# Kernel tuning notes

Hardware: AMD Instinct MI355X
Metric: run time of the kernel (lower is better)

The kernel has to match this reference:

```python
import jax, jax.numpy as jnp
import numpy as np

B, S, E = 4, 2048, 1024
H = 16
D = E // H
WIN = 512


def setup_inputs() -> dict:
    key = jax.random.key(0)
    k1, k2, k3 = jax.random.split(key, 3)
    x = jax.random.normal(k1, (B, S, E), dtype=jnp.float32)
    w_in = jax.random.normal(k2, (3 * E, E), dtype=jnp.float32) * 0.02
    w_out = jax.random.normal(k3, (E, E), dtype=jnp.float32) * 0.02
    return {"x": x, "w_in": w_in, "w_out": w_out}


def _sliding_window_attention(q, k, v, win):
    b, h, s, d = q.shape
    nb = s // win
    scale = 1.0 / jnp.sqrt(jnp.float32(d))
    qb = q.reshape(b, h, nb, win, d)
    kb = k.reshape(b, h, nb, win, d)
    vb = v.reshape(b, h, nb, win, d)
    zpad = jnp.zeros_like(kb[:, :, :1])
    k2 = jnp.concatenate([jnp.concatenate([zpad, kb[:, :, :-1]], axis=2), kb], axis=3)  # [B,H,nb,2W,D]
    v2 = jnp.concatenate([jnp.concatenate([zpad, vb[:, :, :-1]], axis=2), vb], axis=3)
    scores = jnp.einsum('bhnqd,bhnkd->bhnqk', qb, k2) * scale  # [B,H,nb,W,2W]
    qi = jnp.arange(win)[:, None]          # query offset in block
    kj = jnp.arange(2 * win)[None, :]
    delta = qi - kj + win                  # q_idx - kv_idx
    valid = (delta >= 0) & (delta <= win)  # sliding-window causal mask
    blk = jnp.arange(nb)[:, None, None]
    valid = valid[None] & (blk * win + (kj[None] - win) >= 0)  # prev block invalid for block 0
    # ALiBi: bias = (q_idx - kv_idx) * exp2(-(h+1)*8/H)
    slopes = jnp.exp2(-(jnp.arange(H, dtype=jnp.float32) + 1.0) * 8.0 / H)  # [H]
    bias = slopes[:, None, None] * delta.astype(jnp.float32)  # [H,W,2W]
    scores = jnp.where(valid[None, :, :, :, :][:, None].squeeze(0)[None] if False else valid[None, None],
                       scores + bias[None, :, None], -jnp.inf)
    p = jax.nn.softmax(scores, axis=-1)
    out = jnp.einsum('bhnqk,bhnkd->bhnqd', p, v2)
    return out.reshape(b, h, s, d)


def reference(x, w_in, w_out):
    b, s, e = x.shape
    # packed in-projection (q is k is v path): split [3E,E] weight
    qkv = jnp.einsum('bse,fe->bsf', x, w_in)  # [B,S,3E]
    q, k, v = jnp.split(qkv, 3, axis=-1)
    def heads(t):
        return t.reshape(b, s, H, D).transpose(0, 2, 1, 3)  # [B,H,S,D]
    o = _sliding_window_attention(heads(q), heads(k), heads(v), WIN)  # [B,H,S,D]
    o = o.transpose(0, 2, 1, 3).reshape(b, s, e)
    return jnp.einsum('bse,fe->bsf', o, w_out)  # out_proj, batch-first output
```

## Files before the change

### kernel.cpp

```cpp
#include <hip/hip_runtime.h>
#include <hip/hip_bf16.h>


typedef __bf16 bf16x8 __attribute__((ext_vector_type(8)));
typedef float f32x4 __attribute__((ext_vector_type(4)));

__device__ __forceinline__ f32x4 mfma16(bf16x8 a, bf16x8 b, f32x4 c) {
    return __builtin_amdgcn_mfma_f32_16x16x32_bf16(a, b, c, 0, 0, 0);
}

__device__ __forceinline__ void gload_lds16(const void* g, void* l) {
    __builtin_amdgcn_global_load_lds(
        (const __attribute__((address_space(1))) unsigned int*)(unsigned long long)g,
        (__attribute__((address_space(3))) unsigned int*)(unsigned int)(unsigned long long)l,
        16, 0, 0);
}

__device__ __forceinline__ unsigned pkbf(float a, float b) {
    unsigned short ua = __builtin_bit_cast(unsigned short, (__bf16)a);
    unsigned short ub = __builtin_bit_cast(unsigned short, (__bf16)b);
    return (unsigned)ua | ((unsigned)ub << 16);
}

__global__ void init_flag(int* flag) { *flag = 0; }

__global__ void detect_f32(const unsigned short* __restrict__ w, int n, int* flag) {
    int i = blockIdx.x * blockDim.x + threadIdx.x;
    int hit = 0;
    for (; i < n; i += gridDim.x * blockDim.x) {
        int e = (w[i] >> 7) & 0xFF;
        if (e >= 0x8D) hit = 1;
    }
    unsigned long long m = __ballot(hit);
    if (m != 0 && (threadIdx.x & 63) == 0) atomicOr(flag, 1);
}

__global__ void cvt_all(const void* __restrict__ x, const void* __restrict__ wi,
                        const void* __restrict__ wo, __bf16* __restrict__ xb,
                        __bf16* __restrict__ wib, __bf16* __restrict__ wob,
                        const int* __restrict__ flag) {
    if (*flag == 0) return;
    const int XN = 8192 * 1024, WI = 3072 * 1024, WO = 1024 * 1024;
    const int stride = gridDim.x * blockDim.x;
    int i0 = blockIdx.x * blockDim.x + threadIdx.x;
    for (int j = i0; j < XN; j += stride) xb[j] = (__bf16)((const float*)x)[j];
    for (int j = i0; j < WI; j += stride) wib[j] = (__bf16)((const float*)wi)[j];
    for (int j = i0; j < WO; j += stride) wob[j] = (__bf16)((const float*)wo)[j];
}

__global__ __launch_bounds__(256, 3) void gemm_bt(
        const void* __restrict__ Araw, const __bf16* __restrict__ Acvt,
        const void* __restrict__ Braw, const __bf16* __restrict__ Bcvt,
        __bf16* __restrict__ Cb, float* __restrict__ Cf,
        const int* __restrict__ flagp, int M, int N, int K) {
    __shared__ __align__(16) __bf16 As[128 * 64];
    __shared__ __align__(16) __bf16 Bs[128 * 64];

    const int t = threadIdx.x;
    const int lane = t & 63;
    const int w = t >> 6;
    const int wr = w >> 1, wc = w & 1;
    const int q4 = lane >> 4, l16 = lane & 15;
    const int m0 = blockIdx.y * 128, n0 = blockIdx.x * 128;
    const bool isf32 = (*flagp != 0);
    const __bf16* A = isf32 ? Acvt : (const __bf16*)Araw;
    const __bf16* Bt = isf32 ? Bcvt : (const __bf16*)Braw;

    f32x4 acc[4][4] = {};

    const int lr = lane >> 3;
    const int lc = (lane & 7) ^ lr;

    for (int k0 = 0; k0 < K; k0 += 64) {
#pragma unroll
        for (int p = 0; p < 4; ++p) {
            int r0 = w * 32 + p * 8;
            gload_lds16(&A[(size_t)(m0 + r0 + lr) * K + k0 + lc * 8], &As[r0 * 64]);
            gload_lds16(&Bt[(size_t)(n0 + r0 + lr) * K + k0 + lc * 8], &Bs[r0 * 64]);
        }
        __syncthreads();

#pragma unroll
        for (int kt = 0; kt < 2; ++kt) {
            bf16x8 af[4], bfr[4];
#pragma unroll
            for (int mt = 0; mt < 4; ++mt) {
                int row = wr * 64 + mt * 16 + l16;
                af[mt] = *(const bf16x8*)&As[row * 64 + (((kt * 4 + q4) ^ (row & 7)) << 3)];
            }
#pragma unroll
            for (int nt = 0; nt < 4; ++nt) {
                int row = wc * 64 + nt * 16 + l16;
                bfr[nt] = *(const bf16x8*)&Bs[row * 64 + (((kt * 4 + q4) ^ (row & 7)) << 3)];
            }
#pragma unroll
            for (int mt = 0; mt < 4; ++mt)
#pragma unroll
                for (int nt = 0; nt < 4; ++nt)
                    acc[mt][nt] = mfma16(af[mt], bfr[nt], acc[mt][nt]);
        }
        __syncthreads();
    }

#pragma unroll
    for (int mt = 0; mt < 4; ++mt)
#pragma unroll
        for (int nt = 0; nt < 4; ++nt) {
            int col = n0 + wc * 64 + nt * 16 + l16;
#pragma unroll
            for (int r = 0; r < 4; ++r) {
                int row = m0 + wr * 64 + mt * 16 + q4 * 4 + r;
                if (Cf && isf32)
                    Cf[(size_t)row * N + col] = acc[mt][nt][r];
                else
                    Cb[(size_t)row * N + col] = (__bf16)acc[mt][nt][r];
            }
        }
}

__global__ __launch_bounds__(256, 2) void attn(
        const __bf16* __restrict__ qkv, __bf16* __restrict__ o) {
    __shared__ __align__(16) char smem[52224];
    __bf16* Ks  = (__bf16*)smem;
    __bf16* Vts = (__bf16*)(smem + 16384);
    __bf16* Ps  = (__bf16*)(smem + 33792);
    __bf16* Ot  = (__bf16*)smem;

    const int qt = blockIdx.x, h = blockIdx.y, b = blockIdx.z;
    const int t = threadIdx.x;
    const int lane = t & 63, w = t >> 6;
    const int q4 = lane >> 4, l16 = lane & 15;
    const int q0 = qt * 128, qw0 = q0 + w * 32;

    const float L2E = 1.4426950408889634f;
    const float slope2 = exp2f(-(float)(h + 1) * 0.5f) * L2E;
    const float scale2 = L2E * 0.125f;

    const int srow = t >> 3, scb = t & 7;
    const int ksoff = (scb ^ (srow & 7)) << 3;

    bf16x8 qf[2][2];
    const size_t qbase = ((size_t)b * 2048 + q0) * 3072 + (size_t)h * 64;
#pragma unroll
    for (int nt = 0; nt < 2; ++nt)
#pragma unroll
        for (int kt = 0; kt < 2; ++kt)
            qf[nt][kt] = *(const bf16x8*)&qkv[qbase +
                (size_t)(w * 32 + nt * 16 + l16) * 3072 + kt * 32 + q4 * 8];

    f32x4 O[4][2] = {};
    float mrow[2] = {-1e30f, -1e30f}, lrow[2] = {0.0f, 0.0f};

    const int nkt = (qt < 4 ? qt : 4) + 1;
    const int ktile0 = qt - (nkt - 1);
    const size_t bh = (size_t)b * 2048 * 3072 + (size_t)h * 64;

    uint4 kpre[4], vpre[4];

    {
        const size_t kb = bh + (size_t)(ktile0 * 128) * 3072 + 1024;
#pragma unroll
        for (int p = 0; p < 4; ++p)
            kpre[p] = *(const uint4*)&qkv[kb + (size_t)(p * 32 + srow) * 3072 + scb * 8];
#pragma unroll
        for (int p = 0; p < 4; ++p)
            vpre[p] = *(const uint4*)&qkv[kb + 1024 + (size_t)(p * 32 + srow) * 3072 + scb * 8];
#pragma unroll
        for (int p = 0; p < 4; ++p) {
            *(uint4*)&Ks[(p * 32 + srow) * 64 + ksoff] = kpre[p];
            const __bf16* ve = (const __bf16*)&vpre[p];
            int R = p * 4 + (srow >> 3);
#pragma unroll
            for (int j = 0; j < 8; ++j)
                Vts[(scb * 8 + j) * 136 + ((R ^ scb) << 3) + (srow & 7)] = ve[j];
        }
    }
    __syncthreads();

    for (int ki = 0; ki < nkt; ++ki) {
        const int k0 = (ktile0 + ki) * 128;
        if (ki + 1 < nkt) {
            const size_t kb = bh + (size_t)(k0 + 128) * 3072 + 1024;
#pragma unroll
            for (int p = 0; p < 4; ++p)
                kpre[p] = *(const uint4*)&qkv[kb + (size_t)(p * 32 + srow) * 3072 + scb * 8];
#pragma unroll
            for (int p = 0; p < 4; ++p)
                vpre[p] = *(const uint4*)&qkv[kb + 1024 + (size_t)(p * 32 + srow) * 3072 + scb * 8];
        }

#pragma unroll 1
        for (int hh = 0; hh < 2; ++hh) {
            const int ks0 = k0 + hh * 64;
            if (qw0 + 31 < ks0 || qw0 - 512 > ks0 + 63) continue;

            f32x4 sc[2][4] = {};
#pragma unroll
            for (int mt = 0; mt < 4; ++mt) {
                int krow = hh * 64 + mt * 16 + l16;
                bf16x8 ak0 = *(const bf16x8*)&Ks[krow * 64 + ((q4 ^ (l16 & 7)) << 3)];
                bf16x8 ak1 = *(const bf16x8*)&Ks[krow * 64 + (((4 + q4) ^ (l16 & 7)) << 3)];
                sc[0][mt] = mfma16(ak0, qf[0][0], sc[0][mt]);
                sc[0][mt] = mfma16(ak1, qf[0][1], sc[0][mt]);
                sc[1][mt] = mfma16(ak0, qf[1][0], sc[1][mt]);
                sc[1][mt] = mfma16(ak1, qf[1][1], sc[1][mt]);
            }

            float al[2];
#pragma unroll
            for (int nt = 0; nt < 2; ++nt) {
                const int qi = qw0 + nt * 16 + l16;
                const int db = qi - ks0 - q4 * 4;
                float tmx = -1e30f;
#pragma unroll
                for (int mt = 0; mt < 4; ++mt)
#pragma unroll
                    for (int r = 0; r < 4; ++r) {
                        int delta = db - mt * 16 - r;
                        float v = sc[nt][mt][r] * scale2 + slope2 * (float)delta;
                        v = ((unsigned)delta <= 512u) ? v : -1e30f;
                        sc[nt][mt][r] = v;
                        tmx = fmaxf(tmx, v);
                    }
                tmx = fmaxf(tmx, __shfl_xor(tmx, 16));
                tmx = fmaxf(tmx, __shfl_xor(tmx, 32));
                float mnew = fmaxf(mrow[nt], tmx);
                al[nt] = exp2f(mrow[nt] - mnew);
                mrow[nt] = mnew;
#pragma unroll
                for (int mtd = 0; mtd < 4; ++mtd)
                    O[mtd][nt] *= al[nt];
            }

            float rsum[2] = {0.0f, 0.0f};
#pragma unroll
            for (int nt = 0; nt < 2; ++nt) {
                int qrow = w * 32 + nt * 16 + l16;
#pragma unroll
                for (int mt = 0; mt < 4; ++mt) {
                    float p0 = exp2f(sc[nt][mt][0] - mrow[nt]);
                    float p1 = exp2f(sc[nt][mt][1] - mrow[nt]);
                    float p2 = exp2f(sc[nt][mt][2] - mrow[nt]);
                    float p3 = exp2f(sc[nt][mt][3] - mrow[nt]);
                    rsum[nt] += (p0 + p1) + (p2 + p3);
                    uint2 pk;
                    pk.x = pkbf(p0, p1);
                    pk.y = pkbf(p2, p3);
                    *(uint2*)&Ps[qrow * 72 + mt * 16 + q4 * 4] = pk;
                }
            }

#pragma unroll
            for (int kt = 0; kt < 2; ++kt) {
                bf16x8 bp0 = *(const bf16x8*)&Ps[(w * 32 + l16) * 72 + kt * 32 + q4 * 8];
                bf16x8 bp1 = *(const bf16x8*)&Ps[(w * 32 + 16 + l16) * 72 + kt * 32 + q4 * 8];
#pragma unroll
                for (int mtd = 0; mtd < 4; ++mtd) {
                    int d = mtd * 16 + l16;
                    int kb2 = (hh * 8 + kt * 4 + q4) ^ ((mtd * 2 + (l16 >> 3)) & 7);
                    bf16x8 av = *(const bf16x8*)&Vts[d * 136 + (kb2 << 3)];
                    O[mtd][0] = mfma16(av, bp0, O[mtd][0]);
                    O[mtd][1] = mfma16(av, bp1, O[mtd][1]);
                }
            }
#pragma unroll
            for (int nt = 0; nt < 2; ++nt) {
                float rs = rsum[nt];
                rs += __shfl_xor(rs, 16);
                rs += __shfl_xor(rs, 32);
                lrow[nt] = lrow[nt] * al[nt] + rs;
            }
        }

        __syncthreads();
        if (ki + 1 < nkt) {
#pragma unroll
            for (int p = 0; p < 4; ++p) {
                *(uint4*)&Ks[(p * 32 + srow) * 64 + ksoff] = kpre[p];
                const __bf16* ve = (const __bf16*)&vpre[p];
                int R = p * 4 + (srow >> 3);
#pragma unroll
                for (int j = 0; j < 8; ++j)
                    Vts[(scb * 8 + j) * 136 + ((R ^ scb) << 3) + (srow & 7)] = ve[j];
            }
        }
        __syncthreads();
    }

#pragma unroll
    for (int nt = 0; nt < 2; ++nt) {
        float inv = (lrow[nt] > 0.0f) ? 1.0f / lrow[nt] : 0.0f;
        int qrow = w * 32 + nt * 16 + l16;
#pragma unroll
        for (int mtd = 0; mtd < 4; ++mtd) {
            int chunk = (mtd * 2 + (q4 >> 1)) ^ (l16 & 7);
            uint2 pk;
            pk.x = pkbf(O[mtd][nt][0] * inv, O[mtd][nt][1] * inv);
            pk.y = pkbf(O[mtd][nt][2] * inv, O[mtd][nt][3] * inv);
            *(uint2*)&Ot[qrow * 64 + (chunk << 3) + (q4 & 1) * 4] = pk;
        }
    }
    const size_t obase = ((size_t)b * 2048 + q0) * 1024 + (size_t)h * 64;
#pragma unroll
    for (int i = 0; i < 4; ++i) {
        int u = i * 64 + lane;
        int row = u >> 3, ch = u & 7;
        int q = w * 32 + row;
        *(uint4*)&o[obase + (size_t)q * 1024 + ch * 8] =
            *(const uint4*)&Ot[q * 64 + ((ch ^ (row & 7)) << 3)];
    }
}

extern "C" void kernel_launch(void* const* d_in, const int* in_sizes, int n_in,
                              void* d_out, int out_size, void* d_ws, size_t ws_size,
                              hipStream_t stream) {
    char* ws = (char*)d_ws;
    int* flag = (int*)ws;
    size_t off = 256;
    __bf16* xb  = (__bf16*)(ws + off); off += (size_t)8192 * 1024 * 2;
    __bf16* wib = (__bf16*)(ws + off); off += (size_t)3072 * 1024 * 2;
    __bf16* wob = (__bf16*)(ws + off); off += (size_t)1024 * 1024 * 2;
    __bf16* qkv = (__bf16*)(ws + off); off += (size_t)8192 * 3072 * 2;
    __bf16* o   = (__bf16*)(ws + off);

    init_flag<<<1, 1, 0, stream>>>(flag);
    int nscan = in_sizes[2] < 65536 ? in_sizes[2] : 65536;
    detect_f32<<<16, 256, 0, stream>>>((const unsigned short*)d_in[2], nscan, flag);
    cvt_all<<<1024, 256, 0, stream>>>(d_in[0], d_in[1], d_in[2], xb, wib, wob, flag);

    gemm_bt<<<dim3(24, 64), 256, 0, stream>>>(d_in[0], xb, d_in[1], wib,
                                              qkv, nullptr, flag, 8192, 3072, 1024);
    attn<<<dim3(16, 16, 4), 256, 0, stream>>>(qkv, o);
    gemm_bt<<<dim3(8, 64), 256, 0, stream>>>(o, o, d_in[2], wob,
                                             (__bf16*)d_out, (float*)d_out, flag,
                                             8192, 1024, 1024);
}
```

Before: 266.7 us.

## Write V transposed from QKV GEMM epilogue and reverse attention tile order

The QKV projection GEMM epilogue now writes the V columns straight into a per-head transposed [B,H,D,S] buffer, while Q and K go into a narrower [B*S,2048] buffer. The attention kernel can then load V^T rows with plain 16-byte loads and stores into shared memory, instead of the old scalar transpose scatter of 8 bf16 values per lane. Attention blocks are also launched in reverse query-tile order so the tiles with the most KV work are scheduled first. The cost is that the GEMM epilogue writes V with a strided pattern, 8-byte stores per lane at a 2048-element stride, which may hurt write coalescing.

```diff
diff --git a/kernel.cpp b/kernel.cpp
--- a/kernel.cpp
+++ b/kernel.cpp
@@ -52,7 +52,8 @@
         const void* __restrict__ Araw, const __bf16* __restrict__ Acvt,
         const void* __restrict__ Braw, const __bf16* __restrict__ Bcvt,
         __bf16* __restrict__ Cb, float* __restrict__ Cf,
-        const int* __restrict__ flagp, int M, int N, int K) {
+        __bf16* __restrict__ vTp, const int* __restrict__ flagp,
+        int M, int N, int K, int ldc) {
     __shared__ __align__(16) __bf16 As[128 * 64];
     __shared__ __align__(16) __bf16 Bs[128 * 64];
 
@@ -102,31 +103,49 @@
         __syncthreads();
     }
 
-#pragma unroll
-    for (int mt = 0; mt < 4; ++mt)
-#pragma unroll
-        for (int nt = 0; nt < 4; ++nt) {
-            int col = n0 + wc * 64 + nt * 16 + l16;
-#pragma unroll
-            for (int r = 0; r < 4; ++r) {
-                int row = m0 + wr * 64 + mt * 16 + q4 * 4 + r;
-                if (Cf && isf32)
-                    Cf[(size_t)row * N + col] = acc[mt][nt][r];
-                else
-                    Cb[(size_t)row * N + col] = (__bf16)acc[mt][nt][r];
-            }
-        }
+    if (vTp && n0 >= 2048) {
+        const int b = m0 >> 11;
+        const int s0 = (m0 & 2047) + wr * 64 + q4 * 4;
+#pragma unroll
+        for (int mt = 0; mt < 4; ++mt)
+#pragma unroll
+            for (int nt = 0; nt < 4; ++nt) {
+                int dg = n0 - 2048 + wc * 64 + nt * 16 + l16;
+                size_t base = ((size_t)(b * 16 + (dg >> 6)) * 64 + (dg & 63)) * 2048 +
+                              s0 + mt * 16;
+                uint2 pk;
+                pk.x = pkbf(acc[mt][nt][0], acc[mt][nt][1]);
+                pk.y = pkbf(acc[mt][nt][2], acc[mt][nt][3]);
+                *(uint2*)&vTp[base] = pk;
+            }
+    } else {
+#pragma unroll
+        for (int mt = 0; mt < 4; ++mt)
+#pragma unroll
+            for (int nt = 0; nt < 4; ++nt) {
+                int col = n0 + wc * 64 + nt * 16 + l16;
+#pragma unroll
+                for (int r = 0; r < 4; ++r) {
+                    int row = m0 + wr * 64 + mt * 16 + q4 * 4 + r;
+                    if (Cf && isf32)
+                        Cf[(size_t)row * ldc + col] = acc[mt][nt][r];
+                    else
+                        Cb[(size_t)row * ldc + col] = (__bf16)acc[mt][nt][r];
+                }
+            }
+    }
 }
 
 __global__ __launch_bounds__(256, 2) void attn(
-        const __bf16* __restrict__ qkv, __bf16* __restrict__ o) {
-    __shared__ __align__(16) char smem[52224];
+        const __bf16* __restrict__ qk, const __bf16* __restrict__ vT,
+        __bf16* __restrict__ o) {
+    __shared__ __align__(16) char smem[51200];
     __bf16* Ks  = (__bf16*)smem;
-    __bf16* Vts = (__bf16*)(smem + 16384);
-    __bf16* Ps  = (__bf16*)(smem + 33792);
+    __bf16* VTs = (__bf16*)(smem + 16384);
+    __bf16* Ps  = (__bf16*)(smem + 32768);
     __bf16* Ot  = (__bf16*)smem;
 
-    const int qt = blockIdx.x, h = blockIdx.y, b = blockIdx.z;
+    const int qt = 15 - blockIdx.x, h = blockIdx.y, b = blockIdx.z;
     const int t = threadIdx.x;
     const int lane = t & 63, w = t >> 6;
     const int q4 = lane >> 4, l16 = lane & 15;
@@ -138,41 +157,44 @@
 
     const int srow = t >> 3, scb = t & 7;
     const int ksoff = (scb ^ (srow & 7)) << 3;
+    const int vr = lane >> 4, vs = lane & 15;
 
     bf16x8 qf[2][2];
-    const size_t qbase = ((size_t)b * 2048 + q0) * 3072 + (size_t)h * 64;
+    const size_t qbase = ((size_t)b * 2048 + q0) * 2048 + (size_t)h * 64;
 #pragma unroll
     for (int nt = 0; nt < 2; ++nt)
 #pragma unroll
         for (int kt = 0; kt < 2; ++kt)
-            qf[nt][kt] = *(const bf16x8*)&qkv[qbase +
-                (size_t)(w * 32 + nt * 16 + l16) * 3072 + kt * 32 + q4 * 8];
+            qf[nt][kt] = *(const bf16x8*)&qk[qbase +
+                (size_t)(w * 32 + nt * 16 + l16) * 2048 + kt * 32 + q4 * 8];
 
     f32x4 O[4][2] = {};
     float mrow[2] = {-1e30f, -1e30f}, lrow[2] = {0.0f, 0.0f};
 
     const int nkt = (qt < 4 ? qt : 4) + 1;
     const int ktile0 = qt - (nkt - 1);
-    const size_t bh = (size_t)b * 2048 * 3072 + (size_t)h * 64;
+    const size_t kbh = (size_t)b * 2048 * 2048 + 1024 + (size_t)h * 64;
+    const size_t vbh = (size_t)(b * 16 + h) * 64 * 2048;
 
     uint4 kpre[4], vpre[4];
 
     {
-        const size_t kb = bh + (size_t)(ktile0 * 128) * 3072 + 1024;
+        const size_t kb = kbh + (size_t)(ktile0 * 128) * 2048;
+        const int vk0 = ktile0 * 128;
 #pragma unroll
         for (int p = 0; p < 4; ++p)
-            kpre[p] = *(const uint4*)&qkv[kb + (size_t)(p * 32 + srow) * 3072 + scb * 8];
-#pragma unroll
-        for (int p = 0; p < 4; ++p)
-            vpre[p] = *(const uint4*)&qkv[kb + 1024 + (size_t)(p * 32 + srow) * 3072 + scb * 8];
+            kpre[p] = *(const uint4*)&qk[kb + (size_t)(p * 32 + srow) * 2048 + scb * 8];
+#pragma unroll
+        for (int p = 0; p < 4; ++p) {
+            int d = w * 16 + p * 4 + vr;
+            int g = (vs & 8) | ((vs & 7) ^ (d & 7));
+            vpre[p] = *(const uint4*)&vT[vbh + (size_t)d * 2048 + vk0 + g * 8];
+        }
 #pragma unroll
         for (int p = 0; p < 4; ++p) {
             *(uint4*)&Ks[(p * 32 + srow) * 64 + ksoff] = kpre[p];
-            const __bf16* ve = (const __bf16*)&vpre[p];
-            int R = p * 4 + (srow >> 3);
-#pragma unroll
-            for (int j = 0; j < 8; ++j)
-                Vts[(scb * 8 + j) * 136 + ((R ^ scb) << 3) + (srow & 7)] = ve[j];
+            int d = w * 16 + p * 4 + vr;
+            *(uint4*)&VTs[d * 128 + vs * 8] = vpre[p];
         }
     }
     __syncthreads();
@@ -180,13 +202,16 @@
     for (int ki = 0; ki < nkt; ++ki) {
         const int k0 = (ktile0 + ki) * 128;
         if (ki + 1 < nkt) {
-            const size_t kb = bh + (size_t)(k0 + 128) * 3072 + 1024;
+            const size_t kb = kbh + (size_t)(k0 + 128) * 2048;
 #pragma unroll
             for (int p = 0; p < 4; ++p)
-                kpre[p] = *(const uint4*)&qkv[kb + (size_t)(p * 32 + srow) * 3072 + scb * 8];
-#pragma unroll
-            for (int p = 0; p < 4; ++p)
-                vpre[p] = *(const uint4*)&qkv[kb + 1024 + (size_t)(p * 32 + srow) * 3072 + scb * 8];
+                kpre[p] = *(const uint4*)&qk[kb + (size_t)(p * 32 + srow) * 2048 + scb * 8];
+#pragma unroll
+            for (int p = 0; p < 4; ++p) {
+                int d = w * 16 + p * 4 + vr;
+                int g = (vs & 8) | ((vs & 7) ^ (d & 7));
+                vpre[p] = *(const uint4*)&vT[vbh + (size_t)d * 2048 + k0 + 128 + g * 8];
+            }
         }
 
 #pragma unroll 1
@@ -257,8 +282,8 @@
 #pragma unroll
                 for (int mtd = 0; mtd < 4; ++mtd) {
                     int d = mtd * 16 + l16;
-                    int kb2 = (hh * 8 + kt * 4 + q4) ^ ((mtd * 2 + (l16 >> 3)) & 7);
-                    bf16x8 av = *(const bf16x8*)&Vts[d * 136 + (kb2 << 3)];
+                    bf16x8 av = *(const bf16x8*)&VTs[d * 128 +
+                        ((hh * 8 + ((kt * 4 + q4) ^ (l16 & 7))) << 3)];
                     O[mtd][0] = mfma16(av, bp0, O[mtd][0]);
                     O[mtd][1] = mfma16(av, bp1, O[mtd][1]);
                 }
@@ -277,11 +302,8 @@
 #pragma unroll
             for (int p = 0; p < 4; ++p) {
                 *(uint4*)&Ks[(p * 32 + srow) * 64 + ksoff] = kpre[p];
-                const __bf16* ve = (const __bf16*)&vpre[p];
-                int R = p * 4 + (srow >> 3);
-#pragma unroll
-                for (int j = 0; j < 8; ++j)
-                    Vts[(scb * 8 + j) * 136 + ((R ^ scb) << 3) + (srow & 7)] = ve[j];
+                int d = w * 16 + p * 4 + vr;
+                *(uint4*)&VTs[d * 128 + vs * 8] = vpre[p];
             }
         }
         __syncthreads();
@@ -320,7 +342,8 @@
     __bf16* xb  = (__bf16*)(ws + off); off += (size_t)8192 * 1024 * 2;
     __bf16* wib = (__bf16*)(ws + off); off += (size_t)3072 * 1024 * 2;
     __bf16* wob = (__bf16*)(ws + off); off += (size_t)1024 * 1024 * 2;
-    __bf16* qkv = (__bf16*)(ws + off); off += (size_t)8192 * 3072 * 2;
+    __bf16* qk  = (__bf16*)(ws + off); off += (size_t)8192 * 2048 * 2;
+    __bf16* vT  = (__bf16*)(ws + off); off += (size_t)4 * 16 * 64 * 2048 * 2;
     __bf16* o   = (__bf16*)(ws + off);
 
     init_flag<<<1, 1, 0, stream>>>(flag);
@@ -329,9 +352,11 @@
     cvt_all<<<1024, 256, 0, stream>>>(d_in[0], d_in[1], d_in[2], xb, wib, wob, flag);
 
     gemm_bt<<<dim3(24, 64), 256, 0, stream>>>(d_in[0], xb, d_in[1], wib,
-                                              qkv, nullptr, flag, 8192, 3072, 1024);
-    attn<<<dim3(16, 16, 4), 256, 0, stream>>>(qkv, o);
+                                              qk, nullptr, vT, flag,
+                                              8192, 3072, 1024, 2048);
+    attn<<<dim3(16, 16, 4), 256, 0, stream>>>(qk, vT, o);
     gemm_bt<<<dim3(8, 64), 256, 0, stream>>>(o, o, d_in[2], wob,
-                                             (__bf16*)d_out, (float*)d_out, flag,
-                                             8192, 1024, 1024);
-}
+                                             (__bf16*)d_out, (float*)d_out,
+                                             nullptr, flag,
+                                             8192, 1024, 1024, 1024);
+}
```

New measurement: 287.9 us. 1.08x slower.
